# Performance work log

Measured on AMD Instinct MI355X. Metric: run time of the kernel, lower is better.

Reference implementation:

```python
import jax, jax.numpy as jnp
import numpy as np

WS = 7          # window size
NH = 12         # attention heads
D_STATE = 64    # mamba d_state
HEADDIM = 64    # mamba headdim


def layernorm(x, w, b):
    mu = jnp.mean(x, axis=-1, keepdims=True)
    var = jnp.mean((x - mu) ** 2, axis=-1, keepdims=True)
    return (x - mu) * jax.lax.rsqrt(var + 1e-5) * w + b


def mamba2(x, W_in, conv_w, conv_b, dt_bias, A_log, D, mnorm_w, W_out):
    # Mamba2 (SSD) forward: in_proj -> causal depthwise conv+silu -> selective scan -> gated RMSNorm -> out_proj
    B, L, dm = x.shape
    nheads = dt_bias.shape[0]
    d_inner = nheads * HEADDIM
    zxbcdt = x @ W_in                                   # (B,L,2*d_inner+2*d_state+nheads)
    z = zxbcdt[..., :d_inner]
    xBC = zxbcdt[..., d_inner:2 * d_inner + 2 * D_STATE]
    dt = zxbcdt[..., -nheads:]
    conv_dim = xBC.shape[-1]
    pad = conv_w.shape[-1] - 1
    xBC_t = jnp.swapaxes(xBC, 1, 2)                     # (B, conv_dim, L)
    conv_out = jax.lax.conv_general_dilated(
        xBC_t, conv_w[:, None, :], window_strides=(1,), padding=[(pad, 0)],
        feature_group_count=conv_dim, dimension_numbers=('NCH', 'OIH', 'NCH'))
    xBC = jax.nn.silu(jnp.swapaxes(conv_out, 1, 2) + conv_b)
    xs = xBC[..., :d_inner]
    Bm = xBC[..., d_inner:d_inner + D_STATE]            # (B,L,n)
    Cm = xBC[..., d_inner + D_STATE:]                   # (B,L,n)
    dt = jax.nn.softplus(dt + dt_bias)                  # (B,L,h)
    A = -jnp.exp(A_log)                                 # (h,)
    dA = jnp.exp(dt * A)                                # (B,L,h)
    xh = xs.reshape(B, L, nheads, HEADDIM)              # (B,L,h,p)

    def step(h, inp):
        dA_t, dt_t, x_t, B_t, C_t = inp                 # (B,h),(B,h),(B,h,p),(B,n),(B,n)
        dBx = (dt_t[..., None] * x_t)[..., None] * B_t[:, None, None, :]
        h = h * dA_t[..., None, None] + dBx             # (B,h,p,n)
        y = jnp.einsum('bhpn,bn->bhp', h, C_t)
        return h, y

    sw = lambda a: jnp.swapaxes(a, 0, 1)                # time-major
    h0 = jnp.zeros((B, nheads, HEADDIM, D_STATE), x.dtype)
    _, ys = jax.lax.scan(step, h0, (sw(dA), sw(dt), sw(xh), sw(Bm), sw(Cm)))
    y = jnp.swapaxes(ys, 0, 1) + D[None, None, :, None] * xh   # (B,L,h,p)
    y = y.reshape(B, L, d_inner)
    g = y * jax.nn.silu(z)                              # gated RMSNorm (norm_before_gate=False)
    g = g * jax.lax.rsqrt(jnp.mean(g * g, axis=-1, keepdims=True) + 1e-5) * mnorm_w
    return g @ W_out


def gated_window_attention(xw, qkv_w, qkv_b, gate_w, gate_b, proj_w, proj_b):
    B_, N, C = xw.shape
    hd = C // NH
    qkv = (xw @ qkv_w + qkv_b).reshape(B_, N, 3, NH, hd).transpose(2, 0, 3, 1, 4)
    q, k, v = qkv[0] * (hd ** -0.5), qkv[1], qkv[2]     # (B_,h,N,d)
    attn = jax.nn.softmax(jnp.einsum('bhnd,bhmd->bhnm', q, k), axis=-1)
    xa = jnp.einsum('bhnm,bhmd->bhnd', attn, v).transpose(0, 2, 1, 3)  # (B_,N,h,d)
    gate = jax.nn.sigmoid(xw @ gate_w + gate_b)[..., None]             # (B_,N,h,1)
    xa = (xa * gate).reshape(B_, N, C)
    return xa @ proj_w + proj_b


def lgs_forward(x, norm1_w, norm1_b, W_in, conv_w, conv_b, dt_bias, A_log, D, mnorm_w, W_out,
                qkv_w, qkv_b, gate_w, gate_b, proj_w, proj_b, fusion_w, fusion_b,
                norm2_w, norm2_b, fc1_w, fc1_b, fc2_w, fc2_b, H, W):
    B, L, C = x.shape
    shortcut = x
    xn = layernorm(x, norm1_w, norm1_b)
    # Branch A: Mamba2 global scan
    x_mamba = mamba2(xn, W_in, conv_w, conv_b, dt_bias, A_log, D, mnorm_w, W_out)
    # Branch B: gated window attention (shift_size=0 -> no roll, no mask)
    x2d = xn.reshape(B, H, W, C)
    xw = x2d.reshape(B, H // WS, WS, W // WS, WS, C).transpose(0, 1, 3, 2, 4, 5).reshape(-1, WS * WS, C)
    aw = gated_window_attention(xw, qkv_w, qkv_b, gate_w, gate_b, proj_w, proj_b)
    x_attn = aw.reshape(B, H // WS, W // WS, WS, WS, C).transpose(0, 1, 3, 2, 4, 5).reshape(B, L, C)
    # Fuse branches with 1x1 conv (== linear on channel dim)
    x_cat = jnp.concatenate([x_mamba, x_attn], axis=-1)   # (B,L,2C)
    x_fused = x_cat @ fusion_w + fusion_b
    x = shortcut + x_fused
    xn2 = layernorm(x, norm2_w, norm2_b)
    mlp = jax.nn.gelu(xn2 @ fc1_w + fc1_b, approximate=False) @ fc2_w + fc2_b
    return x + mlp


def setup_inputs() -> dict:
    key = jax.random.key(0)
    ks = jax.random.split(key, 16)
    B, H, W, C = 8, 56, 56, 384
    L = H * W
    d_inner, d_state, nheads_m, d_conv = 768, 64, 12, 4
    d_in_proj = 2 * d_inner + 2 * d_state + nheads_m   # 1676
    conv_dim = d_inner + 2 * d_state                   # 896
    s = 0.02
    return {
        'x': jax.random.normal(ks[0], (B, L, C), jnp.float32),
        'norm1_w': jnp.ones((C,), jnp.float32),
        'norm1_b': jnp.zeros((C,), jnp.float32),
        'W_in': jax.random.normal(ks[1], (C, d_in_proj), jnp.float32) * s,
        'conv_w': jax.random.normal(ks[2], (conv_dim, d_conv), jnp.float32) * 0.1,
        'conv_b': jnp.zeros((conv_dim,), jnp.float32),
        'dt_bias': jax.random.normal(ks[3], (nheads_m,), jnp.float32) * 0.5,
        'A_log': jnp.log(jax.random.uniform(ks[4], (nheads_m,), jnp.float32, 1.0, 16.0)),
        'D': jnp.ones((nheads_m,), jnp.float32),
        'mnorm_w': jnp.ones((d_inner,), jnp.float32),
        'W_out': jax.random.normal(ks[5], (d_inner, C), jnp.float32) * s,
        'qkv_w': jax.random.normal(ks[6], (C, 3 * C), jnp.float32) * s,
        'qkv_b': jnp.zeros((3 * C,), jnp.float32),
        'gate_w': jax.random.normal(ks[7], (C, NH), jnp.float32) * s,
        'gate_b': jnp.zeros((NH,), jnp.float32),
        'proj_w': jax.random.normal(ks[8], (C, C), jnp.float32) * s,
        'proj_b': jnp.zeros((C,), jnp.float32),
        'fusion_w': jax.random.normal(ks[9], (2 * C, C), jnp.float32) * s,
        'fusion_b': jnp.zeros((C,), jnp.float32),
        'norm2_w': jnp.ones((C,), jnp.float32),
        'norm2_b': jnp.zeros((C,), jnp.float32),
        'fc1_w': jax.random.normal(ks[10], (C, 4 * C), jnp.float32) * s,
        'fc1_b': jnp.zeros((4 * C,), jnp.float32),
        'fc2_w': jax.random.normal(ks[11], (4 * C, C), jnp.float32) * s,
        'fc2_b': jnp.zeros((C,), jnp.float32),
        'H': H,
        'W': W,
    }


def reference(x, norm1_w, norm1_b, W_in, conv_w, conv_b, dt_bias, A_log, D, mnorm_w, W_out,
              qkv_w, qkv_b, gate_w, gate_b, proj_w, proj_b, fusion_w, fusion_b,
              norm2_w, norm2_b, fc1_w, fc1_b, fc2_w, fc2_b, H, W):
    return lgs_forward(x, norm1_w, norm1_b, W_in, conv_w, conv_b, dt_bias, A_log, D, mnorm_w, W_out,
                       qkv_w, qkv_b, gate_w, gate_b, proj_w, proj_b, fusion_w, fusion_b,
                       norm2_w, norm2_b, fc1_w, fc1_b, fc2_w, fc2_b, H, W)
```

## Files before the change

### kernel.cpp

```cpp
#include <hip/hip_runtime.h>
#include <math.h>

static constexpr int L_SEQ  = 3136;
static constexpr int NBATCH = 8;
static constexpr int CDIM   = 384;
static constexpr int DIN    = 768;
static constexpr int NHM    = 12;
static constexpr int HDM    = 64;
static constexpr int DPROJ  = 1676;
static constexpr int CONVD  = 896;
static constexpr int NROWS  = NBATCH * L_SEQ;
static constexpr int NHA    = 12;
static constexpr int NCH    = 49;
static constexpr int CHT    = 64;
static constexpr int CTK    = 28;

typedef __attribute__((ext_vector_type(8))) short short8;
typedef __attribute__((ext_vector_type(8))) unsigned short ushort8;
typedef __attribute__((ext_vector_type(4))) float f32x4;
typedef const unsigned int __attribute__((address_space(1)))* gua_t;
typedef unsigned int __attribute__((address_space(3)))* lua_t;

__device__ __forceinline__ float siluf(float x) { return x / (1.f + __expf(-x)); }
__device__ __forceinline__ unsigned short f2bf(float f) {
  unsigned int u = __float_as_uint(f);
  u += 0x7fff + ((u >> 16) & 1);
  return (unsigned short)(u >> 16);
}
__device__ __forceinline__ float bf2f(unsigned short h) {
  return __uint_as_float(((unsigned int)h) << 16);
}
__device__ __forceinline__ float fast_erff(float x) {
  float ax = fabsf(x);
  float tt = 1.f / (1.f + 0.3275911f * ax);
  float y = tt * (0.254829592f + tt * (-0.284496736f + tt * (1.421413741f +
            tt * (-1.453152027f + tt * 1.061405429f))));
  float r = 1.f - y * __expf(-ax * ax);
  return copysignf(r, x);
}

__global__ __launch_bounds__(256) void ln_kernel(const float* __restrict__ in,
    const float* __restrict__ w, const float* __restrict__ b, unsigned short* __restrict__ out) {
  int wave = threadIdx.x >> 6, lane = threadIdx.x & 63;
  int row = blockIdx.x * 4 + wave;
  if (row >= NROWS) return;
  const float* r = in + (size_t)row * CDIM;
  float2 v[3];
  float s1 = 0.f, s2 = 0.f;
#pragma unroll
  for (int q = 0; q < 3; q++) {
    v[q] = *(const float2*)&r[q * 128 + lane * 2];
    s1 += v[q].x + v[q].y;
    s2 += v[q].x * v[q].x + v[q].y * v[q].y;
  }
#pragma unroll
  for (int o = 32; o > 0; o >>= 1) { s1 += __shfl_xor(s1, o, 64); s2 += __shfl_xor(s2, o, 64); }
  float mu = s1 * (1.f / 384.f);
  float var = s2 * (1.f / 384.f) - mu * mu;
  float rs = rsqrtf(var + 1e-5f);
  unsigned short* o = out + (size_t)row * CDIM;
#pragma unroll
  for (int q = 0; q < 3; q++) {
    int c = q * 128 + lane * 2;
    float2 wv = *(const float2*)&w[c];
    float2 bv = *(const float2*)&b[c];
    float ox = (v[q].x - mu) * rs * wv.x + bv.x;
    float oy = (v[q].y - mu) * rs * wv.y + bv.y;
    unsigned int pk = (unsigned int)f2bf(ox) | ((unsigned int)f2bf(oy) << 16);
    *(unsigned int*)&o[c] = pk;
  }
}

__global__ __launch_bounds__(256) void wconv_kernel(const float* __restrict__ W,
    unsigned short* __restrict__ WT, int K, int N, int ldw) {
  __shared__ float tile[32][33];
  int k0 = blockIdx.x * 32, n0 = blockIdx.y * 32;
  int tx = threadIdx.x & 31, ty = threadIdx.x >> 5;
#pragma unroll
  for (int j = 0; j < 4; j++) {
    int k = k0 + ty + j * 8;
    int n = n0 + tx;
    tile[ty + j * 8][tx] = (n < N) ? W[(size_t)k * ldw + n] : 0.f;
  }
  __syncthreads();
#pragma unroll
  for (int j = 0; j < 4; j++) {
    int n = n0 + ty + j * 8;
    int k = k0 + tx;
    WT[(size_t)n * K + k] = f2bf(tile[tx][ty + j * 8]);
  }
}

template<int ACT, bool HASBIAS, bool HASRES, bool OUTBF>
__global__ __launch_bounds__(256) void gemm_bf(
    const unsigned short* __restrict__ A, const unsigned short* __restrict__ WT,
    void* __restrict__ Cp, const float* __restrict__ bias,
    const float* __restrict__ res, int ldr,
    int M, int N, int K, int lda, int ldc, int coff)
{
  __shared__ unsigned short As[3][128][32];
  __shared__ unsigned short Ws[3][128][32];
  int t = threadIdx.x;
  int gx = gridDim.x;
  int nwg = gx * gridDim.y;
  int orig = blockIdx.y * gx + blockIdx.x;
  int qq = nwg >> 3, rr = nwg & 7;
  int xcd = orig & 7, seq = orig >> 3;
  int wgid = (xcd < rr ? xcd * (qq + 1) : rr * (qq + 1) + (xcd - rr) * qq) + seq;
  int m0 = (wgid / gx) * 128, n0 = (wgid % gx) * 128;

  int lane = t & 63, w = t >> 6;
  int wr = (w >> 1) * 64, wc = (w & 1) * 64;
  int fl = lane & 15, kq = lane >> 4;
  int so = ((kq ^ ((lane >> 1) & 3))) * 8;
  f32x4 acc[4][4];
#pragma unroll
  for (int i = 0; i < 4; i++)
#pragma unroll
    for (int j = 0; j < 4; j++) acc[i][j] = (f32x4)0.f;

  auto stage = [&](int buf, int k0) {
#pragma unroll
    for (int j = 0; j < 2; j++) {
      int c = j * 256 + t;
      int row = c >> 2, qs = c & 3;
      int qsrc = qs ^ ((row >> 1) & 3);
      __builtin_amdgcn_global_load_lds(
          (gua_t)&A[(size_t)(m0 + row) * lda + k0 + qsrc * 8],
          (lua_t)&As[buf][0][0] + (size_t)c * 4, 16, 0, 0);
      __builtin_amdgcn_global_load_lds(
          (gua_t)&WT[(size_t)(n0 + row) * K + k0 + qsrc * 8],
          (lua_t)&Ws[buf][0][0] + (size_t)c * 4, 16, 0, 0);
    }
  };

  int nk = K >> 5;
  stage(0, 0);
  int sb = 1, rb = 0;
  for (int ks = 0; ks < nk; ks++) {
    if (ks + 1 < nk) {
      stage(sb, (ks + 1) << 5);
      sb = sb == 2 ? 0 : sb + 1;
      asm volatile("s_waitcnt vmcnt(4)" ::: "memory");
    } else {
      asm volatile("s_waitcnt vmcnt(0)" ::: "memory");
    }
    __builtin_amdgcn_s_barrier();
    asm volatile("" ::: "memory");
    __builtin_amdgcn_sched_barrier(0);
    short8 af[4], bfr[4];
#pragma unroll
    for (int mi = 0; mi < 4; mi++) af[mi] = *(const short8*)&As[rb][wr + mi * 16 + fl][so];
#pragma unroll
    for (int ni = 0; ni < 4; ni++) bfr[ni] = *(const short8*)&Ws[rb][wc + ni * 16 + fl][so];
    rb = rb == 2 ? 0 : rb + 1;
#pragma unroll
    for (int mi = 0; mi < 4; mi++)
#pragma unroll
      for (int ni = 0; ni < 4; ni++)
        acc[mi][ni] = __builtin_amdgcn_mfma_f32_16x16x32_bf16(af[mi], bfr[ni], acc[mi][ni], 0, 0, 0);
  }
  int rbase = (lane >> 4) * 4, cl = lane & 15;
#pragma unroll
  for (int mi = 0; mi < 4; mi++) {
#pragma unroll
    for (int ni = 0; ni < 4; ni++) {
      int n = n0 + wc + ni * 16 + cl;
      if (n >= N) continue;
#pragma unroll
      for (int r = 0; r < 4; r++) {
        int m = m0 + wr + mi * 16 + rbase + r;
        float v = acc[mi][ni][r];
        if (HASBIAS) v += bias[n];
        if (ACT == 1) v = 0.5f * v * (1.f + fast_erff(v * 0.70710678118654752f));
        if (HASRES) v += res[(size_t)m * ldr + n];
        if (OUTBF) ((unsigned short*)Cp)[(size_t)m * ldc + coff + n] = f2bf(v);
        else       ((float*)Cp)[(size_t)m * ldc + coff + n] = v;
      }
    }
  }
}

__global__ void dtprep_kernel(float* __restrict__ DT, const float* __restrict__ dt_bias,
    const float* __restrict__ A_log, float* __restrict__ DA) {
  int idx = blockIdx.x * blockDim.x + threadIdx.x;
  if (idx >= NROWS * NHM) return;
  int h = idx % NHM;
  float v = DT[idx] + dt_bias[h];
  float sp = (v > 20.f) ? v : log1pf(expf(v));
  DT[idx] = sp;
  DA[idx] = -expf(A_log[h]) * sp;
}

__global__ __launch_bounds__(256) void conv_bf_kernel(const unsigned short* __restrict__ xbc,
    const float* __restrict__ cw, const float* __restrict__ cb, unsigned short* __restrict__ XC) {
  int t = blockIdx.x * 256 + threadIdx.x;
  int c8 = t % 112;
  int rg = t / 112;
  int b = rg / 112, lc = rg % 112;
  int l0 = lc * CTK;
  int c0 = c8 * 8;
  float w0[8], w1[8], w2[8], w3[8], bq[8];
#pragma unroll
  for (int i = 0; i < 8; i++) {
    bq[i] = cb[c0 + i];
    float4 w4 = *(const float4*)&cw[(c0 + i) * 4];
    w0[i] = w4.x; w1[i] = w4.y; w2[i] = w4.z; w3[i] = w4.w;
  }
  const unsigned short* base = xbc + (size_t)b * L_SEQ * CONVD + c0;
  unsigned short* obase = XC + (size_t)b * L_SEQ * CONVD + c0;
  ushort8 h0 = (ushort8)0, h1 = (ushort8)0, h2 = (ushort8)0;
  if (l0 >= 3) {
    h0 = *(const ushort8*)&base[(size_t)(l0 - 3) * CONVD];
    h1 = *(const ushort8*)&base[(size_t)(l0 - 2) * CONVD];
    h2 = *(const ushort8*)&base[(size_t)(l0 - 1) * CONVD];
  }
  for (int i = 0; i < CTK; i++) {
    ushort8 cur = *(const ushort8*)&base[(size_t)(l0 + i) * CONVD];
    ushort8 ov;
#pragma unroll
    for (int q = 0; q < 8; q++) {
      float acc = bq[q] + w0[q] * bf2f(h0[q]) + w1[q] * bf2f(h1[q])
                + w2[q] * bf2f(h2[q]) + w3[q] * bf2f(cur[q]);
      ov[q] = f2bf(siluf(acc));
    }
    *(ushort8*)&obase[(size_t)(l0 + i) * CONVD] = ov;
    h0 = h1; h1 = h2; h2 = cur;
  }
}

__global__ __launch_bounds__(256) void mscan1_kernel(const unsigned short* __restrict__ XC,
    const float* __restrict__ dtp, const float* __restrict__ dta,
    float* __restrict__ H, float* __restrict__ QS) {
  __shared__ unsigned short Xt[64 * 72];
  __shared__ unsigned short Bt[64 * 72];
  __shared__ float lcs[64];
  __shared__ float wss[64];
  int ch = blockIdx.x, bh = blockIdx.y;
  int b = bh / NHM, head = bh - b * NHM;
  int t = threadIdx.x;
  int l0 = ch * CHT;
  const unsigned short* xcb = XC + ((size_t)b * L_SEQ + l0) * CONVD;
  if (t < 64) {
    size_t ro = ((size_t)b * L_SEQ + l0 + t) * NHM + head;
    float s = dta[ro];
#pragma unroll
    for (int o = 1; o < 64; o <<= 1) {
      float u = __shfl_up(s, o, 64);
      if (t >= o) s += u;
    }
    float lc63 = __shfl(s, 63, 64);
    lcs[t] = s;
    wss[t] = dtp[ro] * __expf(lc63 - s);
    if (t == 63) QS[bh * NCH + ch] = __expf(s);
  }
  __syncthreads();
#pragma unroll
  for (int it = 0; it < 16; it++) {
    int e = it * 256 + t;
    int j = e >> 6, cc = e & 63;
    const unsigned short* rowp = xcb + (size_t)j * CONVD;
    Xt[cc * 72 + j] = rowp[head * HDM + cc];
    Bt[cc * 72 + j] = f2bf(bf2f(rowp[768 + cc]) * wss[j]);
  }
  __syncthreads();
  int lane = t & 63, w = t >> 6;
  int wr = (w >> 1) * 32, wc = (w & 1) * 32;
  int fl = lane & 15, kq = lane >> 4;
  f32x4 acc[2][2];
#pragma unroll
  for (int i = 0; i < 2; i++)
#pragma unroll
    for (int j = 0; j < 2; j++) acc[i][j] = (f32x4)0.f;
#pragma unroll
  for (int kk = 0; kk < 2; kk++) {
    short8 af[2], bfr[2];
#pragma unroll
    for (int mi = 0; mi < 2; mi++)
      af[mi] = *(const short8*)&Xt[(wr + mi * 16 + fl) * 72 + kk * 32 + kq * 8];
#pragma unroll
    for (int ni = 0; ni < 2; ni++)
      bfr[ni] = *(const short8*)&Bt[(wc + ni * 16 + fl) * 72 + kk * 32 + kq * 8];
#pragma unroll
    for (int mi = 0; mi < 2; mi++)
#pragma unroll
      for (int ni = 0; ni < 2; ni++)
        acc[mi][ni] = __builtin_amdgcn_mfma_f32_16x16x32_bf16(af[mi], bfr[ni], acc[mi][ni], 0, 0, 0);
  }
  float* Hp = H + ((size_t)bh * NCH + ch) * 4096;
  int rbase = kq * 4, cl = fl;
#pragma unroll
  for (int mi = 0; mi < 2; mi++)
#pragma unroll
    for (int ni = 0; ni < 2; ni++)
#pragma unroll
      for (int r = 0; r < 4; r++)
        Hp[(size_t)(wr + mi * 16 + rbase + r) * 64 + wc + ni * 16 + cl] = acc[mi][ni][r];
}

__global__ __launch_bounds__(64) void scomb_kernel(float* __restrict__ H,
    const float* __restrict__ QS) {
  int bh = blockIdx.x;
  int e = (blockIdx.y * 64 + threadIdx.x) * 4;
  float4 cur = make_float4(0.f, 0.f, 0.f, 0.f);
  for (int s = 0; s < NCH; s++) {
    float* Hp = H + ((size_t)bh * NCH + s) * 4096 + e;
    float q = QS[bh * NCH + s];
    float4 tmp = *(float4*)Hp;
    *(float4*)Hp = cur;
    cur.x = q * cur.x + tmp.x;
    cur.y = q * cur.y + tmp.y;
    cur.z = q * cur.z + tmp.z;
    cur.w = q * cur.w + tmp.w;
  }
}

__global__ __launch_bounds__(256) void mscan2_kernel(const unsigned short* __restrict__ XC,
    const float* __restrict__ dtp, const float* __restrict__ dta,
    const float* __restrict__ H, const float* __restrict__ Dp,
    unsigned short* __restrict__ Ybf) {
  __shared__ unsigned short Cs[64 * 72];
  __shared__ unsigned short Bs[64 * 72];
  __shared__ unsigned short Xt[64 * 72];
  __shared__ unsigned short Hs[64 * 72];
  __shared__ unsigned short Ss[64 * 72];
  __shared__ float lcs[64];
  __shared__ float dts[64];
  int ch = blockIdx.x, bh = blockIdx.y;
  int b = bh / NHM, head = bh - b * NHM;
  int t = threadIdx.x;
  int l0 = ch * CHT;
  const unsigned short* xcb = XC + ((size_t)b * L_SEQ + l0) * CONVD;
  const float* Hg = H + ((size_t)bh * NCH + ch) * 4096;
  if (t < 64) {
    size_t ro = ((size_t)b * L_SEQ + l0 + t) * NHM + head;
    float s = dta[ro];
#pragma unroll
    for (int o = 1; o < 64; o <<= 1) {
      float u = __shfl_up(s, o, 64);
      if (t >= o) s += u;
    }
    lcs[t] = s;
    dts[t] = dtp[ro];
  }
#pragma unroll
  for (int it = 0; it < 16; it++) {
    int e = it * 256 + t;
    int j = e >> 6, cc = e & 63;
    const unsigned short* rowp = xcb + (size_t)j * CONVD;
    Xt[cc * 72 + j] = rowp[head * HDM + cc];
    Bs[j * 72 + cc] = rowp[768 + cc];
    Cs[j * 72 + cc] = rowp[832 + cc];
    Hs[j * 72 + cc] = f2bf(Hg[e]);
  }
  __syncthreads();
  int lane = t & 63, w = t >> 6;
  int wr = (w >> 1) * 32, wc = (w & 1) * 32;
  int fl = lane & 15, kq = lane >> 4;
  int rbase = kq * 4, cl = fl;
  f32x4 sacc[2][2];
#pragma unroll
  for (int i = 0; i < 2; i++)
#pragma unroll
    for (int j = 0; j < 2; j++) sacc[i][j] = (f32x4)0.f;
#pragma unroll
  for (int kk = 0; kk < 2; kk++) {
    short8 af[2], bfr[2];
#pragma unroll
    for (int mi = 0; mi < 2; mi++)
      af[mi] = *(const short8*)&Cs[(wr + mi * 16 + fl) * 72 + kk * 32 + kq * 8];
#pragma unroll
    for (int ni = 0; ni < 2; ni++)
      bfr[ni] = *(const short8*)&Bs[(wc + ni * 16 + fl) * 72 + kk * 32 + kq * 8];
#pragma unroll
    for (int mi = 0; mi < 2; mi++)
#pragma unroll
      for (int ni = 0; ni < 2; ni++)
        sacc[mi][ni] = __builtin_amdgcn_mfma_f32_16x16x32_bf16(af[mi], bfr[ni], sacc[mi][ni], 0, 0, 0);
  }
  __syncthreads();
#pragma unroll
  for (int mi = 0; mi < 2; mi++)
#pragma unroll
    for (int ni = 0; ni < 2; ni++)
#pragma unroll
      for (int r = 0; r < 4; r++) {
        int i = wr + mi * 16 + rbase + r;
        int j = wc + ni * 16 + cl;
        float v = (j <= i) ? sacc[mi][ni][r] * dts[j] * __expf(lcs[i] - lcs[j]) : 0.f;
        Ss[i * 72 + j] = f2bf(v);
      }
#pragma unroll
  for (int it = 0; it < 16; it++) {
    int e = it * 256 + t;
    int i = e >> 6, n = e & 63;
    float cv = bf2f(Cs[i * 72 + n]) * __expf(lcs[i]);
    Cs[i * 72 + n] = f2bf(cv);
  }
  __syncthreads();
  f32x4 yacc[2][2];
#pragma unroll
  for (int i = 0; i < 2; i++)
#pragma unroll
    for (int j = 0; j < 2; j++) yacc[i][j] = (f32x4)0.f;
#pragma unroll
  for (int kk = 0; kk < 2; kk++) {
    short8 af[2], bfr[2];
#pragma unroll
    for (int mi = 0; mi < 2; mi++)
      af[mi] = *(const short8*)&Ss[(wr + mi * 16 + fl) * 72 + kk * 32 + kq * 8];
#pragma unroll
    for (int ni = 0; ni < 2; ni++)
      bfr[ni] = *(const short8*)&Xt[(wc + ni * 16 + fl) * 72 + kk * 32 + kq * 8];
#pragma unroll
    for (int mi = 0; mi < 2; mi++)
#pragma unroll
      for (int ni = 0; ni < 2; ni++)
        yacc[mi][ni] = __builtin_amdgcn_mfma_f32_16x16x32_bf16(af[mi], bfr[ni], yacc[mi][ni], 0, 0, 0);
  }
#pragma unroll
  for (int kk = 0; kk < 2; kk++) {
    short8 af[2], bfr[2];
#pragma unroll
    for (int mi = 0; mi < 2; mi++)
      af[mi] = *(const short8*)&Cs[(wr + mi * 16 + fl) * 72 + kk * 32 + kq * 8];
#pragma unroll
    for (int ni = 0; ni < 2; ni++)
      bfr[ni] = *(const short8*)&Hs[(wc + ni * 16 + fl) * 72 + kk * 32 + kq * 8];
#pragma unroll
    for (int mi = 0; mi < 2; mi++)
#pragma unroll
      for (int ni = 0; ni < 2; ni++)
        yacc[mi][ni] = __builtin_amdgcn_mfma_f32_16x16x32_bf16(af[mi], bfr[ni], yacc[mi][ni], 0, 0, 0);
  }
  float Dh = Dp[head];
  unsigned short* yb = Ybf + ((size_t)b * L_SEQ + l0) * DIN + head * HDM;
#pragma unroll
  for (int mi = 0; mi < 2; mi++)
#pragma unroll
    for (int ni = 0; ni < 2; ni++)
#pragma unroll
      for (int r = 0; r < 4; r++) {
        int i = wr + mi * 16 + rbase + r;
        int p = wc + ni * 16 + cl;
        float xval = bf2f(Xt[p * 72 + i]);
        yb[(size_t)i * DIN + p] = f2bf(yacc[mi][ni][r] + Dh * xval);
      }
}

__global__ __launch_bounds__(256) void gate_rms_kernel(unsigned short* __restrict__ Y,
    const unsigned short* __restrict__ Z, const float* __restrict__ mw) {
  int wave = threadIdx.x >> 6, lane = threadIdx.x & 63;
  int row = blockIdx.x * 4 + wave;
  if (row >= NROWS) return;
  unsigned short* y = Y + (size_t)row * DIN;
  const unsigned short* z = Z + (size_t)row * DIN;
  float g[12];
  float ss = 0.f;
#pragma unroll
  for (int q = 0; q < 3; q++) {
    int c = q * 256 + lane * 4;
    uint2 yu = *(const uint2*)&y[c];
    uint2 zu = *(const uint2*)&z[c];
    float y0 = bf2f((unsigned short)(yu.x & 0xffff));
    float y1 = bf2f((unsigned short)(yu.x >> 16));
    float y2 = bf2f((unsigned short)(yu.y & 0xffff));
    float y3 = bf2f((unsigned short)(yu.y >> 16));
    float z0 = bf2f((unsigned short)(zu.x & 0xffff));
    float z1 = bf2f((unsigned short)(zu.x >> 16));
    float z2 = bf2f((unsigned short)(zu.y & 0xffff));
    float z3 = bf2f((unsigned short)(zu.y >> 16));
    float g0 = y0 * siluf(z0), g1 = y1 * siluf(z1);
    float g2 = y2 * siluf(z2), g3 = y3 * siluf(z3);
    ss += g0 * g0 + g1 * g1 + g2 * g2 + g3 * g3;
    g[q * 4 + 0] = g0; g[q * 4 + 1] = g1; g[q * 4 + 2] = g2; g[q * 4 + 3] = g3;
  }
#pragma unroll
  for (int o = 32; o > 0; o >>= 1) ss += __shfl_xor(ss, o, 64);
  float rs = rsqrtf(ss * (1.f / 768.f) + 1e-5f);
#pragma unroll
  for (int q = 0; q < 3; q++) {
    int c = q * 256 + lane * 4;
    float4 m = *(const float4*)&mw[c];
    unsigned int lo = (unsigned int)f2bf(g[q*4+0] * rs * m.x) | ((unsigned int)f2bf(g[q*4+1] * rs * m.y) << 16);
    unsigned int hi = (unsigned int)f2bf(g[q*4+2] * rs * m.z) | ((unsigned int)f2bf(g[q*4+3] * rs * m.w) << 16);
    uint2 pk; pk.x = lo; pk.y = hi;
    *(uint2*)&y[c] = pk;
  }
}

__global__ __launch_bounds__(256) void attgate_kernel(const unsigned short* __restrict__ XN,
    const float* __restrict__ gw, const float* __restrict__ gb, float* __restrict__ G) {
  int wave = threadIdx.x >> 6, lane = threadIdx.x & 63;
  int row = blockIdx.x * 4 + wave;
  if (row >= NROWS) return;
  const unsigned short* x = XN + (size_t)row * CDIM;
  float acc[12] = {};
#pragma unroll
  for (int q = 0; q < 6; q++) {
    int k = q * 64 + lane;
    float xv = bf2f(x[k]);
    const float* wr = gw + (size_t)k * 12;
    float4 w0 = *(const float4*)&wr[0];
    float4 w1 = *(const float4*)&wr[4];
    float4 w2 = *(const float4*)&wr[8];
    acc[0] += xv * w0.x; acc[1] += xv * w0.y; acc[2]  += xv * w0.z; acc[3]  += xv * w0.w;
    acc[4] += xv * w1.x; acc[5] += xv * w1.y; acc[6]  += xv * w1.z; acc[7]  += xv * w1.w;
    acc[8] += xv * w2.x; acc[9] += xv * w2.y; acc[10] += xv * w2.z; acc[11] += xv * w2.w;
  }
#pragma unroll
  for (int h = 0; h < 12; h++)
#pragma unroll
    for (int o = 32; o > 0; o >>= 1) acc[h] += __shfl_xor(acc[h], o, 64);
  if (lane == 0) {
#pragma unroll
    for (int h = 0; h < 12; h++) {
      float v = acc[h] + gb[h];
      G[(size_t)row * 12 + h] = 1.f / (1.f + expf(-v));
    }
  }
}

__global__ __launch_bounds__(64) void attn_kernel(const unsigned short* __restrict__ QKV,
    const float* __restrict__ G, unsigned short* __restrict__ XA) {
  __shared__ unsigned short Pl[64 * 72];
  __shared__ unsigned short Vt[32 * 72];
  int blk = blockIdx.x;
  int head = blk % NHA;
  int win = blk / NHA;
  int b = win >> 6;
  int wrw = win & 63;
  int wy = wrw >> 3, wx = wrw & 7;
  int lane = threadIdx.x;
  int fl = lane & 15, kq = lane >> 4;
  const float scale = 0.17677669529663688f;
  size_t bbase = (size_t)b * L_SEQ;
  const unsigned short* qb = QKV + head * 32;

  short8 aq[4], bk[4];
#pragma unroll
  for (int ti = 0; ti < 4; ti++) {
    int tok = ti * 16 + fl; if (tok > 48) tok = 48;
    int iy = tok / 7, ix = tok - iy * 7;
    size_t r = bbase + (size_t)(wy * 7 + iy) * 56 + wx * 7 + ix;
    aq[ti] = *(const short8*)&qb[r * 1152 + kq * 8];
    bk[ti] = *(const short8*)&qb[r * 1152 + 384 + kq * 8];
  }
#pragma unroll
  for (int it = 0; it < 4; it++) {
    int j = (lane >> 2) + it * 16;
    int dc = (lane & 3) * 8;
    ushort8 v8 = (ushort8)0;
    if (j <= 48) {
      int iy = j / 7, ix = j - iy * 7;
      size_t r = bbase + (size_t)(wy * 7 + iy) * 56 + wx * 7 + ix;
      v8 = *(const ushort8*)&qb[r * 1152 + 768 + dc];
    }
#pragma unroll
    for (int q2 = 0; q2 < 8; q2++) {
      int d = dc + q2;
      Vt[d * 72 + (((j >> 3) ^ (d >> 3)) << 3) + (j & 7)] = v8[q2];
    }
  }
  f32x4 sacc[4][4];
#pragma unroll
  for (int tj = 0; tj < 4; tj++)
#pragma unroll
    for (int ti = 0; ti < 4; ti++)
      sacc[tj][ti] = __builtin_amdgcn_mfma_f32_16x16x32_bf16(bk[tj], aq[ti], (f32x4)0.f, 0, 0, 0);
#pragma unroll
  for (int ti = 0; ti < 4; ti++) {
    float mx = -1e30f;
#pragma unroll
    for (int tj = 0; tj < 4; tj++)
#pragma unroll
      for (int r = 0; r < 4; r++) {
        int j = tj * 16 + kq * 4 + r;
        float v = (j < 49) ? sacc[tj][ti][r] * scale : -1e30f;
        sacc[tj][ti][r] = v;
        mx = fmaxf(mx, v);
      }
    mx = fmaxf(mx, __shfl_xor(mx, 16, 64));
    mx = fmaxf(mx, __shfl_xor(mx, 32, 64));
    float sum = 0.f;
#pragma unroll
    for (int tj = 0; tj < 4; tj++)
#pragma unroll
      for (int r = 0; r < 4; r++) {
        float e = __expf(sacc[tj][ti][r] - mx);
        sacc[tj][ti][r] = e;
        sum += e;
      }
    sum += __shfl_xor(sum, 16, 64);
    sum += __shfl_xor(sum, 32, 64);
    float inv = 1.f / sum;
    int i = ti * 16 + fl;
#pragma unroll
    for (int tj = 0; tj < 4; tj++)
#pragma unroll
      for (int r = 0; r < 4; r++) {
        int j = tj * 16 + kq * 4 + r;
        Pl[i * 72 + j] = f2bf(sacc[tj][ti][r] * inv);
      }
  }
  f32x4 oacc[4][2];
#pragma unroll
  for (int i2 = 0; i2 < 4; i2++)
#pragma unroll
    for (int nd = 0; nd < 2; nd++) oacc[i2][nd] = (f32x4)0.f;
#pragma unroll
  for (int kk = 0; kk < 2; kk++) {
    short8 ap[4], bv[2];
#pragma unroll
    for (int i2 = 0; i2 < 4; i2++)
      ap[i2] = *(const short8*)&Pl[(i2 * 16 + fl) * 72 + kk * 32 + kq * 8];
#pragma unroll
    for (int nd = 0; nd < 2; nd++) {
      int d = nd * 16 + fl;
      bv[nd] = *(const short8*)&Vt[d * 72 + (((kk * 4 + kq) ^ (d >> 3)) << 3)];
    }
#pragma unroll
    for (int i2 = 0; i2 < 4; i2++)
#pragma unroll
      for (int nd = 0; nd < 2; nd++)
        oacc[i2][nd] = __builtin_amdgcn_mfma_f32_16x16x32_bf16(ap[i2], bv[nd], oacc[i2][nd], 0, 0, 0);
  }
#pragma unroll
  for (int i2 = 0; i2 < 4; i2++) {
#pragma unroll
    for (int r = 0; r < 4; r++) {
      int i = i2 * 16 + kq * 4 + r;
      if (i > 48) continue;
      int iy = i / 7, ix = i - iy * 7;
      size_t rg = bbase + (size_t)(wy * 7 + iy) * 56 + wx * 7 + ix;
      float g = G[rg * 12 + head];
#pragma unroll
      for (int nd = 0; nd < 2; nd++)
        XA[rg * CDIM + head * 32 + nd * 16 + fl] = f2bf(oacc[i2][nd][r] * g);
    }
  }
}

extern "C" void kernel_launch(void* const* d_in, const int* in_sizes, int n_in,
                              void* d_out, int out_size, void* d_ws, size_t ws_size,
                              hipStream_t stream) {
  const float* x        = (const float*)d_in[0];
  const float* norm1_w  = (const float*)d_in[1];
  const float* norm1_b  = (const float*)d_in[2];
  const float* W_in     = (const float*)d_in[3];
  const float* conv_w   = (const float*)d_in[4];
  const float* conv_b   = (const float*)d_in[5];
  const float* dt_bias  = (const float*)d_in[6];
  const float* A_log    = (const float*)d_in[7];
  const float* Dp       = (const float*)d_in[8];
  const float* mnorm_w  = (const float*)d_in[9];
  const float* W_out    = (const float*)d_in[10];
  const float* qkv_w    = (const float*)d_in[11];
  const float* qkv_b    = (const float*)d_in[12];
  const float* gate_w   = (const float*)d_in[13];
  const float* gate_b   = (const float*)d_in[14];
  const float* proj_w   = (const float*)d_in[15];
  const float* proj_b   = (const float*)d_in[16];
  const float* fusion_w = (const float*)d_in[17];
  const float* fusion_b = (const float*)d_in[18];
  const float* norm2_w  = (const float*)d_in[19];
  const float* norm2_b  = (const float*)d_in[20];
  const float* fc1_w    = (const float*)d_in[21];
  const float* fc1_b    = (const float*)d_in[22];
  const float* fc2_w    = (const float*)d_in[23];
  const float* fc2_b    = (const float*)d_in[24];
  float* OUT = (float*)d_out;

  float* ws = (float*)d_ws;
  unsigned short* XNBF = (unsigned short*)ws;
  float* XC_  = ws + 4816896;
  float* SCR  = XC_ + 22478848;
  unsigned short* YBF = (unsigned short*)(SCR + 22478848);
  unsigned short* WT  = (unsigned short*)(SCR + 22478848 + 9633792);
  float* DT_ = (float*)(WT + 3047424);
  float* DA_ = DT_ + 301056;
  float* G_  = DA_ + 301056;
  float* QS_ = G_  + 301056;

  unsigned short* XBCBF = (unsigned short*)SCR;
  unsigned short* XCBF  = (unsigned short*)XC_;
  float* H_ = SCR;
  unsigned short* ZBF   = (unsigned short*)SCR;
  unsigned short* QKVBF = (unsigned short*)SCR;
  unsigned short* M1BF  = (unsigned short*)SCR;
  unsigned short* CATBF = (unsigned short*)XC_;
  unsigned short* XABF  = (unsigned short*)(XC_ + 9633792);

  unsigned short* wt_xbc  = WT;
  unsigned short* wt_dt   = WT + 344064;
  unsigned short* wt_z    = WT + 393216;
  unsigned short* wt_out  = WT + 688128;
  unsigned short* wt_qkv  = WT + 983040;
  unsigned short* wt_proj = WT + 1425408;
  unsigned short* wt_fus  = WT + 1572864;
  unsigned short* wt_fc1  = WT + 1867776;
  unsigned short* wt_fc2  = WT + 2457600;

  wconv_kernel<<<dim3(12,  28), 256, 0, stream>>>(W_in + 768,  wt_xbc,  384,  896, DPROJ);
  wconv_kernel<<<dim3(12,   4), 256, 0, stream>>>(W_in + 1664, wt_dt,   384,   12, DPROJ);
  wconv_kernel<<<dim3(12,  24), 256, 0, stream>>>(W_in,        wt_z,    384,  768, DPROJ);
  wconv_kernel<<<dim3(24,  12), 256, 0, stream>>>(W_out,       wt_out,  768,  384, 384);
  wconv_kernel<<<dim3(12,  36), 256, 0, stream>>>(qkv_w,       wt_qkv,  384, 1152, 1152);
  wconv_kernel<<<dim3(12,  12), 256, 0, stream>>>(proj_w,      wt_proj, 384,  384, 384);
  wconv_kernel<<<dim3(24,  12), 256, 0, stream>>>(fusion_w,    wt_fus,  768,  384, 384);
  wconv_kernel<<<dim3(12,  48), 256, 0, stream>>>(fc1_w,       wt_fc1,  384, 1536, 1536);
  wconv_kernel<<<dim3(48,  12), 256, 0, stream>>>(fc2_w,       wt_fc2, 1536,  384, 384);

  ln_kernel<<<6272, 256, 0, stream>>>(x, norm1_w, norm1_b, XNBF);

  gemm_bf<0, false, false, true><<<dim3(7, 196), 256, 0, stream>>>(
      XNBF, wt_xbc, XBCBF, nullptr, nullptr, 0, NROWS, CONVD, CDIM, CDIM, CONVD, 0);
  conv_bf_kernel<<<392, 256, 0, stream>>>(XBCBF, conv_w, conv_b, XCBF);
  gemm_bf<0, false, false, false><<<dim3(1, 196), 256, 0, stream>>>(
      XNBF, wt_dt, DT_, nullptr, nullptr, 0, NROWS, NHM, CDIM, CDIM, NHM, 0);

  dtprep_kernel<<<(NROWS * NHM + 255) / 256, 256, 0, stream>>>(DT_, dt_bias, A_log, DA_);

  mscan1_kernel<<<dim3(NCH, 96), 256, 0, stream>>>(XCBF, DT_, DA_, H_, QS_);
  scomb_kernel<<<dim3(96, 16), 64, 0, stream>>>(H_, QS_);
  mscan2_kernel<<<dim3(NCH, 96), 256, 0, stream>>>(XCBF, DT_, DA_, H_, Dp, YBF);

  gemm_bf<0, false, false, true><<<dim3(6, 196), 256, 0, stream>>>(
      XNBF, wt_z, ZBF, nullptr, nullptr, 0, NROWS, DIN, CDIM, CDIM, DIN, 0);
  gate_rms_kernel<<<6272, 256, 0, stream>>>(YBF, ZBF, mnorm_w);

  gemm_bf<0, false, false, true><<<dim3(3, 196), 256, 0, stream>>>(
      YBF, wt_out, CATBF, nullptr, nullptr, 0, NROWS, CDIM, DIN, DIN, 2 * CDIM, 0);

  attgate_kernel<<<6272, 256, 0, stream>>>(XNBF, gate_w, gate_b, G_);

  gemm_bf<0, true, false, true><<<dim3(9, 196), 256, 0, stream>>>(
      XNBF, wt_qkv, QKVBF, qkv_b, nullptr, 0, NROWS, 3 * CDIM, CDIM, CDIM, 3 * CDIM, 0);
  attn_kernel<<<512 * NHA, 64, 0, stream>>>(QKVBF, G_, XABF);

  gemm_bf<0, true, false, true><<<dim3(3, 196), 256, 0, stream>>>(
      XABF, wt_proj, CATBF, proj_b, nullptr, 0, NROWS, CDIM, CDIM, CDIM, 2 * CDIM, CDIM);

  gemm_bf<0, true, true, false><<<dim3(3, 196), 256, 0, stream>>>(
      CATBF, wt_fus, OUT, fusion_b, x, CDIM, NROWS, CDIM, 2 * CDIM, 2 * CDIM, CDIM, 0);

  ln_kernel<<<6272, 256, 0, stream>>>(OUT, norm2_w, norm2_b, XNBF);

  gemm_bf<1, true, false, true><<<dim3(12, 196), 256, 0, stream>>>(
      XNBF, wt_fc1, M1BF, fc1_b, nullptr, 0, NROWS, 4 * CDIM, CDIM, CDIM, 4 * CDIM, 0);
  gemm_bf<0, true, true, false><<<dim3(3, 196), 256, 0, stream>>>(
      M1BF, wt_fc2, OUT, fc2_b, OUT, CDIM, NROWS, CDIM, 4 * CDIM, 4 * CDIM, CDIM, 0);
}
```

Measured before the change: 698.4 us.

## Merge xBC and dt projections into one GEMM, restage GEMM pipeline and epilogue

Merges the xBC projection and the dt projection into a single bf16 GEMM that writes a padded 1024-wide buffer. The conv and dtprep kernels now read from that buffer, which removes one GEMM launch and the separate fp32 DT write. The GEMM loop moves from triple to double buffering with incrementing pointers and waitcnt 0 per step, and sets launch_bounds occupancy to 4. The bf16 epilogue stages tiles in LDS for 16-byte coalesced stores. In exchange, dt is rounded to bf16 before softplus, and the epilogue drops the N bound check, so it writes padding columns into the buffer.

```diff
diff --git a/kernel.cpp b/kernel.cpp
--- a/kernel.cpp
+++ b/kernel.cpp
@@ -14,6 +14,7 @@
 static constexpr int NCH    = 49;
 static constexpr int CHT    = 64;
 static constexpr int CTK    = 28;
+static constexpr int ZXLD   = 1024;
 
 typedef __attribute__((ext_vector_type(8))) short short8;
 typedef __attribute__((ext_vector_type(8))) unsigned short ushort8;
@@ -92,14 +93,13 @@
 }
 
 template<int ACT, bool HASBIAS, bool HASRES, bool OUTBF>
-__global__ __launch_bounds__(256) void gemm_bf(
+__global__ __launch_bounds__(256, 4) void gemm_bf(
     const unsigned short* __restrict__ A, const unsigned short* __restrict__ WT,
     void* __restrict__ Cp, const float* __restrict__ bias,
     const float* __restrict__ res, int ldr,
     int M, int N, int K, int lda, int ldc, int coff)
 {
-  __shared__ unsigned short As[3][128][32];
-  __shared__ unsigned short Ws[3][128][32];
+  __shared__ unsigned short SMEM[16384];
   int t = threadIdx.x;
   int gx = gridDim.x;
   int nwg = gx * gridDim.y;
@@ -112,88 +112,121 @@
   int lane = t & 63, w = t >> 6;
   int wr = (w >> 1) * 64, wc = (w & 1) * 64;
   int fl = lane & 15, kq = lane >> 4;
-  int so = ((kq ^ ((lane >> 1) & 3))) * 8;
+  int so = (kq ^ ((lane >> 1) & 3)) * 8;
+
+  int srow = t >> 2, sq = t & 3;
+  int q0 = sq ^ ((srow >> 1) & 3);
+  const unsigned short* pA0 = A  + (size_t)(m0 + srow) * lda + q0 * 8;
+  const unsigned short* pA1 = A  + (size_t)(m0 + 64 + srow) * lda + q0 * 8;
+  const unsigned short* pW0 = WT + (size_t)(n0 + srow) * K + q0 * 8;
+  const unsigned short* pW1 = WT + (size_t)(n0 + 64 + srow) * K + q0 * 8;
+
   f32x4 acc[4][4];
 #pragma unroll
   for (int i = 0; i < 4; i++)
 #pragma unroll
     for (int j = 0; j < 4; j++) acc[i][j] = (f32x4)0.f;
 
-  auto stage = [&](int buf, int k0) {
-#pragma unroll
-    for (int j = 0; j < 2; j++) {
-      int c = j * 256 + t;
-      int row = c >> 2, qs = c & 3;
-      int qsrc = qs ^ ((row >> 1) & 3);
-      __builtin_amdgcn_global_load_lds(
-          (gua_t)&A[(size_t)(m0 + row) * lda + k0 + qsrc * 8],
-          (lua_t)&As[buf][0][0] + (size_t)c * 4, 16, 0, 0);
-      __builtin_amdgcn_global_load_lds(
-          (gua_t)&WT[(size_t)(n0 + row) * K + k0 + qsrc * 8],
-          (lua_t)&Ws[buf][0][0] + (size_t)c * 4, 16, 0, 0);
-    }
+  auto STAGE = [&](int buf) {
+    unsigned short* as = SMEM + buf * 4096;
+    unsigned short* ws = SMEM + 8192 + buf * 4096;
+    __builtin_amdgcn_global_load_lds((gua_t)pA0, (lua_t)as + t * 4, 16, 0, 0);
+    __builtin_amdgcn_global_load_lds((gua_t)pA1, (lua_t)(as + 2048) + t * 4, 16, 0, 0);
+    __builtin_amdgcn_global_load_lds((gua_t)pW0, (lua_t)ws + t * 4, 16, 0, 0);
+    __builtin_amdgcn_global_load_lds((gua_t)pW1, (lua_t)(ws + 2048) + t * 4, 16, 0, 0);
+    pA0 += 32; pA1 += 32; pW0 += 32; pW1 += 32;
   };
 
   int nk = K >> 5;
-  stage(0, 0);
-  int sb = 1, rb = 0;
+  STAGE(0);
+  asm volatile("s_waitcnt vmcnt(0)" ::: "memory");
+  __builtin_amdgcn_s_barrier();
+  asm volatile("" ::: "memory");
+  __builtin_amdgcn_sched_barrier(0);
+  int buf = 0;
   for (int ks = 0; ks < nk; ks++) {
-    if (ks + 1 < nk) {
-      stage(sb, (ks + 1) << 5);
-      sb = sb == 2 ? 0 : sb + 1;
-      asm volatile("s_waitcnt vmcnt(4)" ::: "memory");
-    } else {
-      asm volatile("s_waitcnt vmcnt(0)" ::: "memory");
-    }
-    __builtin_amdgcn_s_barrier();
-    asm volatile("" ::: "memory");
-    __builtin_amdgcn_sched_barrier(0);
+    if (ks + 1 < nk) STAGE(buf ^ 1);
+    const unsigned short* as = SMEM + buf * 4096;
+    const unsigned short* ws = SMEM + 8192 + buf * 4096;
     short8 af[4], bfr[4];
 #pragma unroll
-    for (int mi = 0; mi < 4; mi++) af[mi] = *(const short8*)&As[rb][wr + mi * 16 + fl][so];
-#pragma unroll
-    for (int ni = 0; ni < 4; ni++) bfr[ni] = *(const short8*)&Ws[rb][wc + ni * 16 + fl][so];
-    rb = rb == 2 ? 0 : rb + 1;
+    for (int mi = 0; mi < 4; mi++) af[mi] = *(const short8*)&as[(wr + mi * 16 + fl) * 32 + so];
+#pragma unroll
+    for (int ni = 0; ni < 4; ni++) bfr[ni] = *(const short8*)&ws[(wc + ni * 16 + fl) * 32 + so];
 #pragma unroll
     for (int mi = 0; mi < 4; mi++)
 #pragma unroll
       for (int ni = 0; ni < 4; ni++)
         acc[mi][ni] = __builtin_amdgcn_mfma_f32_16x16x32_bf16(af[mi], bfr[ni], acc[mi][ni], 0, 0, 0);
-  }
-  int rbase = (lane >> 4) * 4, cl = lane & 15;
-#pragma unroll
-  for (int mi = 0; mi < 4; mi++) {
-#pragma unroll
-    for (int ni = 0; ni < 4; ni++) {
-      int n = n0 + wc + ni * 16 + cl;
-      if (n >= N) continue;
-#pragma unroll
-      for (int r = 0; r < 4; r++) {
-        int m = m0 + wr + mi * 16 + rbase + r;
-        float v = acc[mi][ni][r];
-        if (HASBIAS) v += bias[n];
-        if (ACT == 1) v = 0.5f * v * (1.f + fast_erff(v * 0.70710678118654752f));
-        if (HASRES) v += res[(size_t)m * ldr + n];
-        if (OUTBF) ((unsigned short*)Cp)[(size_t)m * ldc + coff + n] = f2bf(v);
-        else       ((float*)Cp)[(size_t)m * ldc + coff + n] = v;
+    if (ks + 1 < nk) {
+      asm volatile("s_waitcnt vmcnt(0)" ::: "memory");
+      __builtin_amdgcn_s_barrier();
+      asm volatile("" ::: "memory");
+      __builtin_amdgcn_sched_barrier(0);
+      buf ^= 1;
+    }
+  }
+  int rbase = kq * 4, cl = fl;
+  if (OUTBF) {
+    __builtin_amdgcn_s_barrier();
+#pragma unroll
+    for (int mi = 0; mi < 4; mi++)
+#pragma unroll
+      for (int ni = 0; ni < 4; ni++) {
+        int n = wc + ni * 16 + cl;
+        float bv = HASBIAS ? bias[n0 + n] : 0.f;
+#pragma unroll
+        for (int r = 0; r < 4; r++) {
+          float v = acc[mi][ni][r] + bv;
+          if (ACT == 1) v = 0.5f * v * (1.f + fast_erff(v * 0.70710678118654752f));
+          SMEM[(wr + mi * 16 + rbase + r) * 128 + n] = f2bf(v);
+        }
       }
-    }
-  }
-}
-
-__global__ void dtprep_kernel(float* __restrict__ DT, const float* __restrict__ dt_bias,
-    const float* __restrict__ A_log, float* __restrict__ DA) {
+    __builtin_amdgcn_s_barrier();
+    unsigned short* outp = (unsigned short*)Cp + coff + n0;
+#pragma unroll
+    for (int it2 = 0; it2 < 8; it2++) {
+      int c = it2 * 256 + t;
+      int rrow = c >> 4, c8 = (c & 15) * 8;
+      ushort8 v8 = *(const ushort8*)&SMEM[rrow * 128 + c8];
+      *(ushort8*)&outp[(size_t)(m0 + rrow) * ldc + c8] = v8;
+    }
+  } else {
+#pragma unroll
+    for (int mi = 0; mi < 4; mi++) {
+#pragma unroll
+      for (int ni = 0; ni < 4; ni++) {
+        int n = n0 + wc + ni * 16 + cl;
+        if (n >= N) continue;
+#pragma unroll
+        for (int r = 0; r < 4; r++) {
+          int m = m0 + wr + mi * 16 + rbase + r;
+          float v = acc[mi][ni][r];
+          if (HASBIAS) v += bias[n];
+          if (ACT == 1) v = 0.5f * v * (1.f + fast_erff(v * 0.70710678118654752f));
+          if (HASRES) v += res[(size_t)m * ldr + n];
+          ((float*)Cp)[(size_t)m * ldc + coff + n] = v;
+        }
+      }
+    }
+  }
+}
+
+__global__ void dtprep_kernel(const unsigned short* __restrict__ ZX, const float* __restrict__ dt_bias,
+    const float* __restrict__ A_log, float* __restrict__ DT, float* __restrict__ DA) {
   int idx = blockIdx.x * blockDim.x + threadIdx.x;
   if (idx >= NROWS * NHM) return;
   int h = idx % NHM;
-  float v = DT[idx] + dt_bias[h];
+  int row = idx / NHM;
+  float v = bf2f(ZX[(size_t)row * ZXLD + 896 + h]) + dt_bias[h];
   float sp = (v > 20.f) ? v : log1pf(expf(v));
   DT[idx] = sp;
   DA[idx] = -expf(A_log[h]) * sp;
 }
 
 __global__ __launch_bounds__(256) void conv_bf_kernel(const unsigned short* __restrict__ xbc,
-    const float* __restrict__ cw, const float* __restrict__ cb, unsigned short* __restrict__ XC) {
+    const float* __restrict__ cw, const float* __restrict__ cb, unsigned short* __restrict__ XC,
+    int ldin) {
   int t = blockIdx.x * 256 + threadIdx.x;
   int c8 = t % 112;
   int rg = t / 112;
@@ -207,16 +240,16 @@
     float4 w4 = *(const float4*)&cw[(c0 + i) * 4];
     w0[i] = w4.x; w1[i] = w4.y; w2[i] = w4.z; w3[i] = w4.w;
   }
-  const unsigned short* base = xbc + (size_t)b * L_SEQ * CONVD + c0;
+  const unsigned short* base = xbc + (size_t)b * L_SEQ * ldin + c0;
   unsigned short* obase = XC + (size_t)b * L_SEQ * CONVD + c0;
   ushort8 h0 = (ushort8)0, h1 = (ushort8)0, h2 = (ushort8)0;
   if (l0 >= 3) {
-    h0 = *(const ushort8*)&base[(size_t)(l0 - 3) * CONVD];
-    h1 = *(const ushort8*)&base[(size_t)(l0 - 2) * CONVD];
-    h2 = *(const ushort8*)&base[(size_t)(l0 - 1) * CONVD];
+    h0 = *(const ushort8*)&base[(size_t)(l0 - 3) * ldin];
+    h1 = *(const ushort8*)&base[(size_t)(l0 - 2) * ldin];
+    h2 = *(const ushort8*)&base[(size_t)(l0 - 1) * ldin];
   }
   for (int i = 0; i < CTK; i++) {
-    ushort8 cur = *(const ushort8*)&base[(size_t)(l0 + i) * CONVD];
+    ushort8 cur = *(const ushort8*)&base[(size_t)(l0 + i) * ldin];
     ushort8 ov;
 #pragma unroll
     for (int q = 0; q < 8; q++) {
@@ -682,7 +715,7 @@
   float* G_  = DA_ + 301056;
   float* QS_ = G_  + 301056;
 
-  unsigned short* XBCBF = (unsigned short*)SCR;
+  unsigned short* ZXBF  = (unsigned short*)SCR;
   unsigned short* XCBF  = (unsigned short*)XC_;
   float* H_ = SCR;
   unsigned short* ZBF   = (unsigned short*)SCR;
@@ -691,8 +724,7 @@
   unsigned short* CATBF = (unsigned short*)XC_;
   unsigned short* XABF  = (unsigned short*)(XC_ + 9633792);
 
-  unsigned short* wt_xbc  = WT;
-  unsigned short* wt_dt   = WT + 344064;
+  unsigned short* wt_xbcdt = WT;
   unsigned short* wt_z    = WT + 393216;
   unsigned short* wt_out  = WT + 688128;
   unsigned short* wt_qkv  = WT + 983040;
@@ -701,8 +733,7 @@
   unsigned short* wt_fc1  = WT + 1867776;
   unsigned short* wt_fc2  = WT + 2457600;
 
-  wconv_kernel<<<dim3(12,  28), 256, 0, stream>>>(W_in + 768,  wt_xbc,  384,  896, DPROJ);
-  wconv_kernel<<<dim3(12,   4), 256, 0, stream>>>(W_in + 1664, wt_dt,   384,   12, DPROJ);
+  wconv_kernel<<<dim3(12,  29), 256, 0, stream>>>(W_in + 768,  wt_xbcdt, 384, 908, DPROJ);
   wconv_kernel<<<dim3(12,  24), 256, 0, stream>>>(W_in,        wt_z,    384,  768, DPROJ);
   wconv_kernel<<<dim3(24,  12), 256, 0, stream>>>(W_out,       wt_out,  768,  384, 384);
   wconv_kernel<<<dim3(12,  36), 256, 0, stream>>>(qkv_w,       wt_qkv,  384, 1152, 1152);
@@ -713,13 +744,10 @@
 
   ln_kernel<<<6272, 256, 0, stream>>>(x, norm1_w, norm1_b, XNBF);
 
-  gemm_bf<0, false, false, true><<<dim3(7, 196), 256, 0, stream>>>(
-      XNBF, wt_xbc, XBCBF, nullptr, nullptr, 0, NROWS, CONVD, CDIM, CDIM, CONVD, 0);
-  conv_bf_kernel<<<392, 256, 0, stream>>>(XBCBF, conv_w, conv_b, XCBF);
-  gemm_bf<0, false, false, false><<<dim3(1, 196), 256, 0, stream>>>(
-      XNBF, wt_dt, DT_, nullptr, nullptr, 0, NROWS, NHM, CDIM, CDIM, NHM, 0);
-
-  dtprep_kernel<<<(NROWS * NHM + 255) / 256, 256, 0, stream>>>(DT_, dt_bias, A_log, DA_);
+  gemm_bf<0, false, false, true><<<dim3(8, 196), 256, 0, stream>>>(
+      XNBF, wt_xbcdt, ZXBF, nullptr, nullptr, 0, NROWS, 908, CDIM, CDIM, ZXLD, 0);
+  conv_bf_kernel<<<392, 256, 0, stream>>>(ZXBF, conv_w, conv_b, XCBF, ZXLD);
+  dtprep_kernel<<<(NROWS * NHM + 255) / 256, 256, 0, stream>>>(ZXBF, dt_bias, A_log, DT_, DA_);
 
   mscan1_kernel<<<dim3(NCH, 96), 256, 0, stream>>>(XCBF, DT_, DA_, H_, QS_);
   scomb_kernel<<<dim3(96, 16), 64, 0, stream>>>(H_, QS_);
```

Result: faster. 656.0 us (-6.1%).
